# Optimization experiments

Hardware: AMD Instinct MI355X
Metric: run time of the kernel (lower is better)

The kernel has to match this reference:

```python
import jax, jax.numpy as jnp
import numpy as np

B, N, D, H, CD = 1, 512, 256, 8, 3
HD = D // H
HID = int(D * 4.0 * (2.0 / 3.0))  # 682, SwiGLU hidden


def _ln(x, w, b, eps=1e-5):
    mu = jnp.mean(x, axis=-1, keepdims=True)
    var = jnp.var(x, axis=-1, keepdims=True)
    return (x - mu) / jnp.sqrt(var + eps) * w + b


def setup_inputs() -> dict:
    key = jax.random.key(0)
    ks = jax.random.split(key, 24)
    g = lambda i, shape, fan: jax.random.normal(ks[i], shape, jnp.float32) * (1.0 / np.sqrt(fan))
    return {
        "x": jax.random.normal(ks[0], (B, N, D), jnp.float32),
        "coords": jax.random.normal(ks[1], (B, N, CD), jnp.float32),
        "ln1_w": jnp.ones((D,), jnp.float32), "ln1_b": jnp.zeros((D,), jnp.float32),
        "ln2_w": jnp.ones((D,), jnp.float32), "ln2_b": jnp.zeros((D,), jnp.float32),
        "qkv_w": g(2, (3 * D, D), D), "qkv_b": jnp.zeros((3 * D,), jnp.float32),
        "rb1_w": g(3, (D, CD), CD), "rb1_b": jnp.zeros((D,), jnp.float32),
        "rb2_w": g(4, (H, D), D), "rb2_b": jnp.zeros((H,), jnp.float32),
        "rv1_w": g(5, (D, CD), CD), "rv1_b": jnp.zeros((D,), jnp.float32),
        "rv2_w": g(6, (D, D), D), "rv2_b": jnp.zeros((D,), jnp.float32),
        "ffn_w1": g(7, (HID, D), D), "ffn_b1": jnp.zeros((HID,), jnp.float32),
        "ffn_w2": g(8, (HID, D), D), "ffn_b2": jnp.zeros((HID,), jnp.float32),
        "ffn_w3": g(9, (D, HID), HID), "ffn_b3": jnp.zeros((D,), jnp.float32),
    }


def _forward(x, coords, ln1_w, ln1_b, ln2_w, ln2_b, qkv_w, qkv_b,
             rb1_w, rb1_b, rb2_w, rb2_b, rv1_w, rv1_b, rv2_w, rv2_b,
             ffn_w1, ffn_b1, ffn_w2, ffn_b2, ffn_w3, ffn_b3):
    silu = jax.nn.silu
    xn = _ln(x, ln1_w, ln1_b)
    qkv = xn @ qkv_w.T + qkv_b                       # [B,N,3D]
    q, k, v = jnp.split(qkv, 3, axis=-1)
    tohead = lambda t: t.reshape(B, N, H, HD).transpose(0, 2, 1, 3)  # [B,H,N,hd]
    qh, kh, vh = tohead(q), tohead(k), tohead(v)

    rel = coords[:, :, None, :] - coords[:, None, :, :]              # [B,N,N,3]
    rel_bias = silu(rel @ rb1_w.T + rb1_b) @ rb2_w.T + rb2_b         # [B,N,N,H]
    rel_bias = rel_bias.transpose(0, 3, 1, 2)                        # [B,H,N,N]
    rel_value = silu(rel @ rv1_w.T + rv1_b) @ rv2_w.T + rv2_b        # [B,N,N,D]
    rel_value = rel_value.reshape(B, N, N, H, HD).transpose(0, 3, 1, 2, 4)  # [B,H,N,N,hd]

    scores = jnp.einsum('bhid,bhjd->bhij', qh, kh) / np.sqrt(float(HD))
    weights = jax.nn.softmax(scores + rel_bias, axis=-1)             # [B,H,N,N]
    context = jnp.einsum('bhij,bhjd->bhid', weights, vh) \
            + jnp.einsum('bhij,bhijd->bhid', weights, rel_value)
    attn_out = context.transpose(0, 2, 1, 3).reshape(B, N, D)

    x = x + attn_out
    xn2 = _ln(x, ln2_w, ln2_b)
    ffn = (silu(xn2 @ ffn_w1.T + ffn_b1) * (xn2 @ ffn_w2.T + ffn_b2)) @ ffn_w3.T + ffn_b3
    return x + ffn


def reference(x, coords, ln1_w, ln1_b, ln2_w, ln2_b, qkv_w, qkv_b,
              rb1_w, rb1_b, rb2_w, rb2_b, rv1_w, rv1_b, rv2_w, rv2_b,
              ffn_w1, ffn_b1, ffn_w2, ffn_b2, ffn_w3, ffn_b3):
    return _forward(x, coords, ln1_w, ln1_b, ln2_w, ln2_b, qkv_w, qkv_b,
                    rb1_w, rb1_b, rb2_w, rb2_b, rv1_w, rv1_b, rv2_w, rv2_b,
                    ffn_w1, ffn_b1, ffn_w2, ffn_b2, ffn_w3, ffn_b3)
```

## Files before the change

kernel.cpp:

```cpp
#include <hip/hip_runtime.h>


#define NN 512
#define DD 256
#define HH 8
#define HIDN 682
#define QKSCALE 0.17677669529663687f

#define OFF_QB    0
#define OFF_PB    65536
#define OFF_X2    0
#define OFF_KF    131072
#define OFF_RB2F  196608
#define OFF_XN2   131072
#define OFF_RV2F  262144
#define OFF_VT    294912
#define OFF_PV    360448
#define OFF_WB    425984
#define OFF_XN    425984
#define OFF_QKVP  557056
#define OFF_W12P  425984
#define OFF_W3P   775168
#define OFF_H1    949760

typedef float  f32x4  __attribute__((ext_vector_type(4)));
typedef short  bf16x8 __attribute__((ext_vector_type(8)));
typedef __fp16 fp16x2 __attribute__((ext_vector_type(2)));
typedef unsigned int u32;

static __device__ __forceinline__ float wredSum(float v){
#pragma unroll
  for (int o = 1; o < 64; o <<= 1) v += __shfl_xor(v, o, 64);
  return v;
}
static __device__ __forceinline__ float wredMax(float v){
#pragma unroll
  for (int o = 1; o < 64; o <<= 1) v = fmaxf(v, __shfl_xor(v, o, 64));
  return v;
}
static __device__ __forceinline__ float fsilu(float x){
  return x * __builtin_amdgcn_rcpf(1.0f + __expf(-x));
}
static __device__ __forceinline__ u32 cvtpk(float lo, float hi){
  u32 d; asm("v_cvt_pk_bf16_f32 %0, %1, %2" : "=v"(d) : "v"(lo), "v"(hi));
  return d;
}
static __device__ __forceinline__ u32 pkf16(float lo, float hi){
  fp16x2 r = __builtin_amdgcn_cvt_pkrtz(lo, hi);
  union{fp16x2 h; u32 u;} c; c.h = r; return c.u;
}
static __device__ __forceinline__ float f16lo(u32 d){
  union{unsigned short s; __fp16 h;} c; c.s = (unsigned short)(d & 0xffffu); return (float)c.h;
}
static __device__ __forceinline__ float f16hi(u32 d){
  union{unsigned short s; __fp16 h;} c; c.s = (unsigned short)(d >> 16); return (float)c.h;
}
static __device__ __forceinline__ bf16x8 mkfrag(u32 a, u32 b, u32 c, u32 d){
  union{u32 u[4]; bf16x8 s;} f; f.u[0]=a; f.u[1]=b; f.u[2]=c; f.u[3]=d; return f.s;
}
static __device__ __forceinline__ float dot4(float4 a, float4 b){
  return a.x*b.x + a.y*b.y + a.z*b.z + a.w*b.w;
}

__global__ __launch_bounds__(256) void k1_prep(
    const float* __restrict__ x, const float* __restrict__ coords,
    const float* __restrict__ ln1_w, const float* __restrict__ ln1_b,
    const float* __restrict__ rb1_w, const float* __restrict__ rv1_w,
    const float* __restrict__ rv2_w, const float* __restrict__ rb2_w,
    const float* __restrict__ qkv_w, float* __restrict__ ws)
{
  __shared__ float r4[4];
  const int b = blockIdx.x, t = threadIdx.x;
  if (b < 512) {
    const int lane = t & 63, wid = t >> 6;
    const float v = x[b*DD + t];
    float s = wredSum(v);
    if (lane == 0) r4[wid] = s;
    __syncthreads();
    const float mu = (r4[0]+r4[1]+r4[2]+r4[3]) * (1.0f/DD);
    const float d = v - mu;
    float s2 = wredSum(d*d);
    __syncthreads();
    if (lane == 0) r4[wid] = s2;
    __syncthreads();
    const float var = (r4[0]+r4[1]+r4[2]+r4[3]) * (1.0f/DD);
    ws[OFF_XN + b*DD + t] = d*rsqrtf(var + 1e-5f)*ln1_w[t] + ln1_b[t];
  } else if (b < 528) {
    u32* PB32 = (u32*)(ws + OFF_PB);
#pragma unroll
    for (int k = 0; k < 4; ++k) {
      const int L = (b-512)*1024 + k*256 + t;
      const int jt = L >> 9, ks = (L >> 6) & 7, ln = L & 63;
      const int lmm = ln & 15, lgg = ln >> 4;
      const int j = jt*16 + lmm, e0 = ks*32 + lgg*8;
      const float c0 = coords[j*3], c1 = coords[j*3+1], c2 = coords[j*3+2];
      float p[8];
#pragma unroll
      for (int r = 0; r < 8; ++r)
        p[r] = c0*rb1_w[(e0+r)*3] + c1*rb1_w[(e0+r)*3+1] + c2*rb1_w[(e0+r)*3+2];
      uint4 q; q.x = pkf16(p[0],p[1]); q.y = pkf16(p[2],p[3]);
      q.z = pkf16(p[4],p[5]); q.w = pkf16(p[6],p[7]);
      *(uint4*)(PB32 + (size_t)L*4) = q;
    }
  } else if (b < 544) {
    u32* PV32 = (u32*)(ws + OFF_PV);
#pragma unroll
    for (int k = 0; k < 4; ++k) {
      const int L = (b-528)*1024 + k*256 + t;
      const int et = L >> 10, ks = (L >> 6) & 15, ln = L & 63;
      const int lmm = ln & 15, lgg = ln >> 4;
      const int e = et*16 + lmm, j0 = ks*32 + lgg*8;
      const float w0 = rv1_w[e*3], w1 = rv1_w[e*3+1], w2 = rv1_w[e*3+2];
      float p[8];
#pragma unroll
      for (int r = 0; r < 8; ++r)
        p[r] = coords[(j0+r)*3]*w0 + coords[(j0+r)*3+1]*w1 + coords[(j0+r)*3+2]*w2;
      uint4 q; q.x = pkf16(p[0],p[1]); q.y = pkf16(p[2],p[3]);
      q.z = pkf16(p[4],p[5]); q.w = pkf16(p[6],p[7]);
      *(uint4*)(PV32 + (size_t)L*4) = q;
    }
  } else if (b < 552) {
    u32* RV32 = (u32*)(ws + OFF_RV2F);
#pragma unroll
    for (int k = 0; k < 4; ++k) {
      const int L = (b-544)*1024 + k*256 + t;
      const int mt = L >> 9, ks2 = (L >> 6) & 7, ln = L & 63;
      const int lmm = ln & 15, lgg = ln >> 4;
      const int c = mt*16 + lmm, e0 = ks2*32 + lgg*8;
      const float4 f0 = *(const float4*)(rv2_w + c*DD + e0);
      const float4 f1 = *(const float4*)(rv2_w + c*DD + e0 + 4);
      uint4 q; q.x = cvtpk(f0.x,f0.y); q.y = cvtpk(f0.z,f0.w);
      q.z = cvtpk(f1.x,f1.y); q.w = cvtpk(f1.z,f1.w);
      *(uint4*)(RV32 + (size_t)L*4) = q;
    }
  } else if (b == 552) {
    u32* RBF = (u32*)(ws + OFF_RB2F);
    const int l = t & 63, lmm = l & 15, lgg = (l >> 4) & 3, kq = t >> 6;
#pragma unroll
    for (int g = 0; g < 2; ++g) {
      const int ks = g*4 + kq;
      u32 dw[4];
#pragma unroll
      for (int dd = 0; dd < 4; ++dd) {
        const int e0 = ks*32 + lgg*8 + 2*dd;
        const float f0 = (lmm < HH) ? rb2_w[lmm*DD + e0]     : 0.f;
        const float f1 = (lmm < HH) ? rb2_w[lmm*DD + e0 + 1] : 0.f;
        dw[dd] = cvtpk(f0, f1);
      }
      uint4 q4; q4.x = dw[0]; q4.y = dw[1]; q4.z = dw[2]; q4.w = dw[3];
      *(uint4*)(RBF + (ks*64 + l)*4) = q4;
    }
  } else {
    float4* dst = (float4*)(ws + OFF_QKVP);
#pragma unroll
    for (int k = 0; k < 4; ++k) {
      const int L4 = (b - 553)*1024 + k*256 + t;
      const int O = L4 % 768, k4 = L4 / 768;
      dst[L4] = *(const float4*)(qkv_w + O*DD + k4*4);
    }
  }
}

__global__ __launch_bounds__(256) void k2_qkv(
    float* __restrict__ ws, const float* __restrict__ qkv_b)
{
  const int i0 = blockIdx.x*2, rep = blockIdx.y, t = threadIdx.x;
  const int O = rep*DD + t;
  const float4* xn4 = (const float4*)(ws + OFF_XN);
  const float4* wp4 = (const float4*)(ws + OFF_QKVP);
  float a0 = qkv_b[O], a1 = a0;
  for (int k4 = 0; k4 < 64; ++k4) {
    const float4 w = wp4[k4*768 + O];
    const float4 x0 = xn4[i0*64 + k4];
    const float4 x1 = xn4[i0*64 + 64 + k4];
    a0 += dot4(x0, w);
    a1 += dot4(x1, w);
  }
  if (rep == 0) {
    u32* QB = (u32*)(ws + OFF_QB);
    const float s0 = a0*QKSCALE, s1 = a1*QKSCALE;
    const float p0 = __shfl_xor(s0, 1);
    const float p1 = __shfl_xor(s1, 1);
    if ((t & 1) == 0) {
      QB[i0*128 + (t >> 1)]     = cvtpk(s0, p0);
      QB[(i0+1)*128 + (t >> 1)] = cvtpk(s1, p1);
    }
  } else if (rep == 1) {
    u32* KF = (u32*)(ws + OFF_KF);
    const float p0 = __shfl_xor(a0, 1);
    const float p1 = __shfl_xor(a1, 1);
    if ((t & 1) == 0) {
      const int hq = t >> 5, lgk = (t >> 3) & 3, dw = (t & 7) >> 1;
      const int jt0_ = i0 >> 4, lm0 = i0 & 15;
      KF[(((jt0_*8 + hq)*4 + lgk)*16 + lm0)*4 + dw] = cvtpk(a0, p0);
      const int j1 = i0 + 1, jt1_ = j1 >> 4, lm1 = j1 & 15;
      KF[(((jt1_*8 + hq)*4 + lgk)*16 + lm1)*4 + dw] = cvtpk(a1, p1);
    }
  } else {
    u32* VT = (u32*)(ws + OFF_VT);
    VT[t*256 + (i0 >> 1)] = cvtpk(a0, a1);
  }
}

__global__ __launch_bounds__(256, 2) void k3a_scores(
    const float* __restrict__ coords, const float* __restrict__ rb1_w,
    const float* __restrict__ rb1_b, float* __restrict__ ws)
{
  __shared__ __align__(16) float aI4[4][DD];
  __shared__ __align__(16) float eI4[4][DD];
  const int bx = blockIdx.x, t = threadIdx.x;
  const int it = bx >> 2, jq = bx & 3, i0 = it*4;
  const int lane = t & 63, w = t >> 6, lm = lane & 15, lg = lane >> 4;
  {
    const float w0 = rb1_w[t*3], w1 = rb1_w[t*3+1], w2 = rb1_w[t*3+2], bb = rb1_b[t];
#pragma unroll
    for (int i = 0; i < 4; ++i) {
      const float a = coords[(i0+i)*3]*w0 + coords[(i0+i)*3+1]*w1
                    + coords[(i0+i)*3+2]*w2 + bb;
      aI4[i][t] = a; eI4[i][t] = __expf(-a);
    }
  }
  __syncthreads();
  const uint4* PBu = (const uint4*)(ws + OFF_PB);
  const uint4* KFu = (const uint4*)(ws + OFF_KF);
  const uint4* QBu = (const uint4*)(ws + OFF_QB);
  const u32*   RBF = (const u32*)(ws + OFF_RB2F);
  const int jtA = jq*8 + w*2;
  f32x4 z = {0,0,0,0};
  f32x4 acc[2][4] = {{z,z,z,z},{z,z,z,z}};
  for (int ks = 0; ks < 8; ++ks) {
    const uint4 bd = *(const uint4*)(RBF + (ks*64 + lane)*4);
    const bf16x8 bfr = mkfrag(bd.x,bd.y,bd.z,bd.w);
    float4 aA[4][2], eA[4][2];
#pragma unroll
    for (int i = 0; i < 4; ++i) {
      aA[i][0] = *(const float4*)&aI4[i][ks*32 + lg*8];
      aA[i][1] = *(const float4*)&aI4[i][ks*32 + lg*8 + 4];
      eA[i][0] = *(const float4*)&eI4[i][ks*32 + lg*8];
      eA[i][1] = *(const float4*)&eI4[i][ks*32 + lg*8 + 4];
    }
#pragma unroll
    for (int j2 = 0; j2 < 2; ++j2) {
      const uint4 pd = PBu[((jtA+j2)*8 + ks)*64 + lane];
      float p[8], ep[8];
      p[0]=f16lo(pd.x); p[1]=f16hi(pd.x); p[2]=f16lo(pd.y); p[3]=f16hi(pd.y);
      p[4]=f16lo(pd.z); p[5]=f16hi(pd.z); p[6]=f16lo(pd.w); p[7]=f16hi(pd.w);
#pragma unroll
      for (int r = 0; r < 8; ++r) ep[r] = __expf(p[r]);
#pragma unroll
      for (int i = 0; i < 4; ++i) {
        const float* aa = (const float*)&aA[i][0];
        const float* ee = (const float*)&eA[i][0];
        float s[8];
#pragma unroll
        for (int r = 0; r < 8; ++r)
          s[r] = (aa[r] - p[r]) * __builtin_amdgcn_rcpf(fmaf(ee[r], ep[r], 1.f));
        const bf16x8 afr = mkfrag(cvtpk(s[0],s[1]), cvtpk(s[2],s[3]),
                                  cvtpk(s[4],s[5]), cvtpk(s[6],s[7]));
        acc[j2][i] = __builtin_amdgcn_mfma_f32_16x16x32_bf16(afr, bfr, acc[j2][i], 0,0,0);
      }
    }
  }
#pragma unroll
  for (int hq = 0; hq < 8; ++hq) {
    uint4 qd[4];
#pragma unroll
    for (int i = 0; i < 4; ++i) qd[i] = QBu[(i0+i)*32 + hq*4 + lg];
    const bool sel = (lm == hq);
#pragma unroll
    for (int j2 = 0; j2 < 2; ++j2) {
      const uint4 kd = KFu[((jtA+j2)*8 + hq)*64 + lane];
      const bf16x8 kfr = mkfrag(kd.x,kd.y,kd.z,kd.w);
#pragma unroll
      for (int i = 0; i < 4; ++i) {
        const bf16x8 qfr = mkfrag(sel?qd[i].x:0u, sel?qd[i].y:0u,
                                  sel?qd[i].z:0u, sel?qd[i].w:0u);
        acc[j2][i] = __builtin_amdgcn_mfma_f32_16x16x32_bf16(kfr, qfr, acc[j2][i], 0,0,0);
      }
    }
  }
  u32* WB = (u32*)(ws + OFF_WB);
  if (lm < HH) {
#pragma unroll
    for (int j2 = 0; j2 < 2; ++j2) {
      const int jt = jtA + j2, j0 = jt*16 + lg*4;
      const int ksw = j0 >> 5, rr = j0 & 31, lgw = rr >> 3, d0 = (rr & 7) >> 1;
#pragma unroll
      for (int i = 0; i < 4; ++i) {
        const int idx = (((i0+i)*16 + ksw)*32 + lgw*8 + lm)*4 + d0;
        uint2 st; st.x = pkf16(acc[j2][i][0], acc[j2][i][1]);
        st.y = pkf16(acc[j2][i][2], acc[j2][i][3]);
        *(uint2*)(WB + idx) = st;
      }
    }
  }
}

__global__ __launch_bounds__(256) void k3b_softmax(float* __restrict__ ws)
{
  const int i = blockIdx.x, t = threadIdx.x;
  const int lane = t & 63, w4 = t >> 6;
  u32* WB = (u32*)(ws + OFF_WB);
  const int ks = lane >> 2, d = lane & 3;
#pragma unroll
  for (int hh = 0; hh < 2; ++hh) {
    const int h = w4 + hh*4;
    u32 dv[4]; float v[8];
#pragma unroll
    for (int lg = 0; lg < 4; ++lg) {
      dv[lg] = WB[(i*16 + ks)*128 + (lg*8 + h)*4 + d];
      v[lg*2]   = f16lo(dv[lg]);
      v[lg*2+1] = f16hi(dv[lg]);
    }
    float m = v[0];
#pragma unroll
    for (int r = 1; r < 8; ++r) m = fmaxf(m, v[r]);
    m = wredMax(m);
    float s = 0.f;
#pragma unroll
    for (int r = 0; r < 8; ++r) { v[r] = __expf(v[r] - m); s += v[r]; }
    s = wredSum(s);
    const float rz = __builtin_amdgcn_rcpf(s);
#pragma unroll
    for (int lg = 0; lg < 4; ++lg)
      WB[(i*16 + ks)*128 + (lg*8 + h)*4 + d] = cvtpk(v[lg*2]*rz, v[lg*2+1]*rz);
  }
}

__global__ __launch_bounds__(512, 2) void k3c_ctx(
    const float* __restrict__ x, const float* __restrict__ coords,
    const float* __restrict__ rv1_w, const float* __restrict__ rv1_b,
    const float* __restrict__ rv2_b, const float* __restrict__ ln2_w,
    const float* __restrict__ ln2_b, float* __restrict__ ws)
{
  __shared__ __align__(16) float aV2[2][DD];
  __shared__ __align__(16) float eV2[2][DD];
  __shared__ __align__(16) float Gs[2][HH][260];
  __shared__ __align__(16) float x2t[2][257];
  __shared__ float red[2][4];
  const int bx = blockIdx.x, t = threadIdx.x, i0 = bx*2;
  const int lane = t & 63, w = t >> 6, lm = lane & 15, lg = lane >> 4;
  {
    const int ii = t >> 8, e = t & 255;
    const float pv = coords[(i0+ii)*3]*rv1_w[e*3] + coords[(i0+ii)*3+1]*rv1_w[e*3+1]
                   + coords[(i0+ii)*3+2]*rv1_w[e*3+2] + rv1_b[e];
    aV2[ii][e] = pv; eV2[ii][e] = __expf(-pv);
  }
  __syncthreads();
  const uint4* WBu = (const uint4*)(ws + OFF_WB);
  const uint4* PVu = (const uint4*)(ws + OFF_PV);
  const uint4* VTu = (const uint4*)(ws + OFF_VT);
  const uint4* RVu = (const uint4*)(ws + OFF_RV2F);
  f32x4 z = {0,0,0,0};
  f32x4 accg[2][2] = {{z,z},{z,z}};
  f32x4 ac1[2] = {z,z};
  float aV[2][2], eV[2][2];
#pragma unroll
  for (int e2 = 0; e2 < 2; ++e2)
#pragma unroll
    for (int ig = 0; ig < 2; ++ig) {
      aV[e2][ig] = aV2[ig][(w*2+e2)*16 + lm];
      eV[e2][ig] = eV2[ig][(w*2+e2)*16 + lm];
    }
  for (int ks = 0; ks < 16; ++ks) {
    bf16x8 wfr[2];
#pragma unroll
    for (int ig = 0; ig < 2; ++ig) {
      const uint4 wd = WBu[((i0+ig)*16 + ks)*32 + lg*8 + lm];
      wfr[ig] = mkfrag(wd.x,wd.y,wd.z,wd.w);
    }
    const uint4 cd = WBu[((i0+lm)*16 + ks)*32 + lg*8 + w];
    const bf16x8 c1b = mkfrag(cd.x,cd.y,cd.z,cd.w);
#pragma unroll
    for (int e2 = 0; e2 < 2; ++e2) {
      const int et = w*2 + e2;
      const uint4 pd = PVu[(et*16 + ks)*64 + lane];
      float p[8], ep[8];
      p[0]=f16lo(pd.x); p[1]=f16hi(pd.x); p[2]=f16lo(pd.y); p[3]=f16hi(pd.y);
      p[4]=f16lo(pd.z); p[5]=f16hi(pd.z); p[6]=f16lo(pd.w); p[7]=f16hi(pd.w);
#pragma unroll
      for (int r = 0; r < 8; ++r) ep[r] = __expf(p[r]);
#pragma unroll
      for (int ig = 0; ig < 2; ++ig) {
        float s[8];
#pragma unroll
        for (int r = 0; r < 8; ++r)
          s[r] = (aV[e2][ig] - p[r]) * __builtin_amdgcn_rcpf(fmaf(eV[e2][ig], ep[r], 1.f));
        const bf16x8 afr = mkfrag(cvtpk(s[0],s[1]), cvtpk(s[2],s[3]),
                                  cvtpk(s[4],s[5]), cvtpk(s[6],s[7]));
        accg[e2][ig] = __builtin_amdgcn_mfma_f32_16x16x32_bf16(afr, wfr[ig], accg[e2][ig], 0,0,0);
      }
    }
#pragma unroll
    for (int m2 = 0; m2 < 2; ++m2) {
      const int c = (w*2 + m2)*16 + lm;
      const uint4 vd = VTu[c*64 + ks*4 + lg];
      const bf16x8 vfr = mkfrag(vd.x,vd.y,vd.z,vd.w);
      ac1[m2] = __builtin_amdgcn_mfma_f32_16x16x32_bf16(vfr, c1b, ac1[m2], 0,0,0);
    }
  }
  if (lm < HH) {
#pragma unroll
    for (int e2 = 0; e2 < 2; ++e2)
#pragma unroll
      for (int ig = 0; ig < 2; ++ig)
#pragma unroll
        for (int g = 0; g < 4; ++g)
          Gs[ig][lm][(w*2+e2)*16 + lg*4 + g] = accg[e2][ig][g];
  }
  __syncthreads();
  f32x4 ac2[2] = {z,z};
  const int il = lm & 1;
  for (int k2 = 0; k2 < 8; ++k2) {
    const float4 g0 = *(const float4*)&Gs[il][w][k2*32 + lg*8];
    const float4 g1 = *(const float4*)&Gs[il][w][k2*32 + lg*8 + 4];
    const bf16x8 gfr = mkfrag(cvtpk(g0.x,g0.y), cvtpk(g0.z,g0.w),
                              cvtpk(g1.x,g1.y), cvtpk(g1.z,g1.w));
#pragma unroll
    for (int m2 = 0; m2 < 2; ++m2) {
      const uint4 ad = RVu[((w*2+m2)*8 + k2)*64 + lane];
      const bf16x8 afr = mkfrag(ad.x,ad.y,ad.z,ad.w);
      ac2[m2] = __builtin_amdgcn_mfma_f32_16x16x32_bf16(afr, gfr, ac2[m2], 0,0,0);
    }
  }
#pragma unroll
  for (int m2 = 0; m2 < 2; ++m2) {
    const int c0 = (w*2 + m2)*16 + lg*4;
    const float4 rb = *(const float4*)(rv2_b + c0);
    if (lm < 2) {
      const float4 xv = *(const float4*)(x + (i0+lm)*DD + c0);
      x2t[lm][c0+0] = ac1[m2][0] + ac2[m2][0] + rb.x + xv.x;
      x2t[lm][c0+1] = ac1[m2][1] + ac2[m2][1] + rb.y + xv.y;
      x2t[lm][c0+2] = ac1[m2][2] + ac2[m2][2] + rb.z + xv.z;
      x2t[lm][c0+3] = ac1[m2][3] + ac2[m2][3] + rb.w + xv.w;
    }
  }
  __syncthreads();
  const int ii = t >> 8, c = t & 255;
  const float v = x2t[ii][c];
  float s1 = wredSum(v);
  if (lane == 0) red[ii][w & 3] = s1;
  __syncthreads();
  const float mu = (red[ii][0]+red[ii][1]+red[ii][2]+red[ii][3]) * (1.0f/DD);
  const float dv = v - mu;
  float s2 = wredSum(dv*dv);
  __syncthreads();
  if (lane == 0) red[ii][w & 3] = s2;
  __syncthreads();
  const float var = (red[ii][0]+red[ii][1]+red[ii][2]+red[ii][3]) * (1.0f/DD);
  const float rstd = rsqrtf(var + 1e-5f);
  ws[OFF_X2  + (i0+ii)*DD + c] = v;
  ws[OFF_XN2 + (i0+ii)*DD + c] = dv*rstd*ln2_w[c] + ln2_b[c];
}

__global__ __launch_bounds__(256) void k3p_pack(
    const float* __restrict__ w1, const float* __restrict__ w2,
    const float* __restrict__ w3, float* __restrict__ ws)
{
  const int b = blockIdx.x, t = threadIdx.x;
  if (b < 88) {
    float4* dst = (float4*)(ws + OFF_W12P);
    for (int L4 = b*256 + t; L4 < 87296; L4 += 88*256) {
      const int pr = L4 & 1, rest = L4 >> 1;
      const int O = rest % 682, k4 = rest / 682;
      dst[L4] = *(const float4*)((pr ? w2 : w1) + O*DD + k4*4);
    }
  } else {
    float2* dst = (float2*)(ws + OFF_W3P);
    for (int L2 = (b-88)*256 + t; L2 < 87296; L2 += 44*256) {
      const int c = L2 & 255, k2i = L2 >> 8;
      dst[L2] = *(const float2*)(w3 + c*HIDN + 2*k2i);
    }
  }
}

__global__ __launch_bounds__(256) void k4_ffn1(
    float* __restrict__ ws, const float* __restrict__ b1, const float* __restrict__ b2)
{
  __shared__ __align__(16) float xr[4][DD];
  const int i0 = blockIdx.x*4, rep = blockIdx.y, t = threadIdx.x;
#pragma unroll
  for (int r = 0; r < 4; ++r) xr[r][t] = ws[OFF_XN2 + (i0+r)*DD + t];
  __syncthreads();
  const int O = rep*DD + t;
  if (O >= HIDN) return;
  const float4* wp4 = (const float4*)(ws + OFF_W12P);
  float a1[4], a2[4];
  const float bb1 = b1[O], bb2 = b2[O];
#pragma unroll
  for (int r = 0; r < 4; ++r) { a1[r] = bb1; a2[r] = bb2; }
  for (int k4 = 0; k4 < 64; ++k4) {
    const float4 u = wp4[(k4*HIDN + O)*2];
    const float4 v = wp4[(k4*HIDN + O)*2 + 1];
#pragma unroll
    for (int r = 0; r < 4; ++r) {
      const float4 xv = *(const float4*)&xr[r][k4*4];
      a1[r] += dot4(xv, u); a2[r] += dot4(xv, v);
    }
  }
#pragma unroll
  for (int r = 0; r < 4; ++r)
    ws[OFF_H1 + (size_t)(i0+r)*HIDN + O] = fsilu(a1[r]) * a2[r];
}

__global__ __launch_bounds__(256) void k5_ffn2(
    const float* __restrict__ ws, const float* __restrict__ b3, float* __restrict__ out)
{
  __shared__ __align__(16) float hr[2][HIDN + 2];
  const int i0 = blockIdx.x*2, c = threadIdx.x;
#pragma unroll
  for (int r = 0; r < 2; ++r)
    for (int e = c; e < HIDN; e += 256)
      hr[r][e] = ws[OFF_H1 + (size_t)(i0+r)*HIDN + e];
  __syncthreads();
  const float2* wp2 = (const float2*)(ws + OFF_W3P);
  float acc0 = b3[c] + ws[OFF_X2 + i0*DD + c];
  float acc1 = b3[c] + ws[OFF_X2 + (i0+1)*DD + c];
  for (int k = 0; k < 341; ++k) {
    const float2 wv = wp2[k*DD + c];
    const float2 h0 = *(const float2*)&hr[0][2*k];
    const float2 h1 = *(const float2*)&hr[1][2*k];
    acc0 += h0.x*wv.x + h0.y*wv.y;
    acc1 += h1.x*wv.x + h1.y*wv.y;
  }
  out[i0*DD + c] = acc0;
  out[(i0+1)*DD + c] = acc1;
}

extern "C" void kernel_launch(void* const* d_in, const int* in_sizes, int n_in,
                              void* d_out, int out_size, void* d_ws, size_t ws_size,
                              hipStream_t stream) {
  (void)in_sizes; (void)n_in; (void)out_size; (void)ws_size;
  const float* x      = (const float*)d_in[0];
  const float* coords = (const float*)d_in[1];
  const float* ln1_w  = (const float*)d_in[2];
  const float* ln1_b  = (const float*)d_in[3];
  const float* ln2_w  = (const float*)d_in[4];
  const float* ln2_b  = (const float*)d_in[5];
  const float* qkv_w  = (const float*)d_in[6];
  const float* qkv_b  = (const float*)d_in[7];
  const float* rb1_w  = (const float*)d_in[8];
  const float* rb1_b  = (const float*)d_in[9];
  const float* rb2_w  = (const float*)d_in[10];
  const float* rv1_w  = (const float*)d_in[12];
  const float* rv1_b  = (const float*)d_in[13];
  const float* rv2_w  = (const float*)d_in[14];
  const float* rv2_b  = (const float*)d_in[15];
  const float* ffn_w1 = (const float*)d_in[16];
  const float* ffn_b1 = (const float*)d_in[17];
  const float* ffn_w2 = (const float*)d_in[18];
  const float* ffn_b2 = (const float*)d_in[19];
  const float* ffn_w3 = (const float*)d_in[20];
  const float* ffn_b3 = (const float*)d_in[21];
  float* ws  = (float*)d_ws;
  float* out = (float*)d_out;

  k1_prep<<<601, 256, 0, stream>>>(x, coords, ln1_w, ln1_b, rb1_w, rv1_w,
                                   rv2_w, rb2_w, qkv_w, ws);
  k2_qkv<<<dim3(256, 3), 256, 0, stream>>>(ws, qkv_b);
  k3a_scores<<<512, 256, 0, stream>>>(coords, rb1_w, rb1_b, ws);
  k3b_softmax<<<512, 256, 0, stream>>>(ws);
  k3c_ctx<<<256, 512, 0, stream>>>(x, coords, rv1_w, rv1_b, rv2_b, ln2_w, ln2_b, ws);
  k3p_pack<<<132, 256, 0, stream>>>(ffn_w1, ffn_w2, ffn_w3, ws);
  k4_ffn1<<<dim3(128, 3), 256, 0, stream>>>(ws, ffn_b1, ffn_b2);
  k5_ffn2<<<256, 256, 0, stream>>>(ws, ffn_b3, out);
}
```

Baseline: 209.0 us.

## Pack QKV and FFN weights as bf16 in prep kernel, drop separate pack kernel

Weights for the QKV projection and the three FFN matrices are converted to bf16 inside the first prep kernel, which replaces the separate FFN pack kernel and removes one launch. The QKV and FFN matmul kernels now read bf16 weights, halving their weight traffic, and unpack them to fp32 for FMA. QKV now handles 4 rows per block staged in shared memory, and FFN1 handles 8 rows per block, so each weight load is reused across more rows. The trade-offs are bf16 rounding of the weights, which may affect accuracy, and a reworked workspace layout that moves several buffers to new offsets.

```diff
diff --git a/kernel.cpp b/kernel.cpp
--- a/kernel.cpp
+++ b/kernel.cpp
@@ -9,19 +9,19 @@
 
 #define OFF_QB    0
 #define OFF_PB    65536
-#define OFF_X2    0
 #define OFF_KF    131072
 #define OFF_RB2F  196608
-#define OFF_XN2   131072
-#define OFF_RV2F  262144
-#define OFF_VT    294912
-#define OFF_PV    360448
-#define OFF_WB    425984
-#define OFF_XN    425984
-#define OFF_QKVP  557056
-#define OFF_W12P  425984
-#define OFF_W3P   775168
-#define OFF_H1    949760
+#define OFF_RV2F  198656
+#define OFF_VT    231424
+#define OFF_PV    296960
+#define OFF_WB    362496
+#define OFF_XN    1443904
+#define OFF_X2    1574976
+#define OFF_XN2   1706048
+#define OFF_H1    1837120
+#define OFF_QKVPB 2186304
+#define OFF_W12B  2284608
+#define OFF_W3B   2459200
 
 typedef float  f32x4  __attribute__((ext_vector_type(4)));
 typedef short  bf16x8 __attribute__((ext_vector_type(8)));
@@ -55,11 +55,14 @@
 static __device__ __forceinline__ float f16hi(u32 d){
   union{unsigned short s; __fp16 h;} c; c.s = (unsigned short)(d >> 16); return (float)c.h;
 }
+static __device__ __forceinline__ float bflo(u32 u){
+  union{u32 v; float f;} c; c.v = u << 16; return c.f;
+}
+static __device__ __forceinline__ float bfhi(u32 u){
+  union{u32 v; float f;} c; c.v = u & 0xffff0000u; return c.f;
+}
 static __device__ __forceinline__ bf16x8 mkfrag(u32 a, u32 b, u32 c, u32 d){
   union{u32 u[4]; bf16x8 s;} f; f.u[0]=a; f.u[1]=b; f.u[2]=c; f.u[3]=d; return f.s;
-}
-static __device__ __forceinline__ float dot4(float4 a, float4 b){
-  return a.x*b.x + a.y*b.y + a.z*b.z + a.w*b.w;
 }
 
 __global__ __launch_bounds__(256) void k1_prep(
@@ -67,7 +70,9 @@
     const float* __restrict__ ln1_w, const float* __restrict__ ln1_b,
     const float* __restrict__ rb1_w, const float* __restrict__ rv1_w,
     const float* __restrict__ rv2_w, const float* __restrict__ rb2_w,
-    const float* __restrict__ qkv_w, float* __restrict__ ws)
+    const float* __restrict__ qkv_w, const float* __restrict__ w1,
+    const float* __restrict__ w2, const float* __restrict__ w3,
+    float* __restrict__ ws)
 {
   __shared__ float r4[4];
   const int b = blockIdx.x, t = threadIdx.x;
@@ -110,11 +115,11 @@
       const int et = L >> 10, ks = (L >> 6) & 15, ln = L & 63;
       const int lmm = ln & 15, lgg = ln >> 4;
       const int e = et*16 + lmm, j0 = ks*32 + lgg*8;
-      const float w0 = rv1_w[e*3], w1 = rv1_w[e*3+1], w2 = rv1_w[e*3+2];
+      const float w0 = rv1_w[e*3], w1_ = rv1_w[e*3+1], w2_ = rv1_w[e*3+2];
       float p[8];
 #pragma unroll
       for (int r = 0; r < 8; ++r)
-        p[r] = coords[(j0+r)*3]*w0 + coords[(j0+r)*3+1]*w1 + coords[(j0+r)*3+2]*w2;
+        p[r] = coords[(j0+r)*3]*w0 + coords[(j0+r)*3+1]*w1_ + coords[(j0+r)*3+2]*w2_;
       uint4 q; q.x = pkf16(p[0],p[1]); q.y = pkf16(p[2],p[3]);
       q.z = pkf16(p[4],p[5]); q.w = pkf16(p[6],p[7]);
       *(uint4*)(PV32 + (size_t)L*4) = q;
@@ -150,13 +155,44 @@
       uint4 q4; q4.x = dw[0]; q4.y = dw[1]; q4.z = dw[2]; q4.w = dw[3];
       *(uint4*)(RBF + (ks*64 + l)*4) = q4;
     }
+  } else if (b < 601) {
+    uint2* qp = (uint2*)(ws + OFF_QKVPB);
+#pragma unroll
+    for (int k = 0; k < 4; ++k) {
+      const int idx = (b-553)*1024 + k*256 + t;
+      const int O = idx % 768, kp = idx / 768;
+      const float4 wv = *(const float4*)(qkv_w + O*DD + kp*4);
+      uint2 u; u.x = cvtpk(wv.x, wv.y); u.y = cvtpk(wv.z, wv.w);
+      qp[idx] = u;
+    }
+  } else if (b < 687) {
+    uint2* wp = (uint2*)(ws + OFF_W12B);
+#pragma unroll
+    for (int k = 0; k < 4; ++k) {
+      const int idx = (b-601)*1024 + k*256 + t;
+      if (idx < 87296) {
+        const int m = idx & 1, r2 = idx >> 1;
+        const int O = r2 % HIDN, kp = r2 / HIDN;
+        const float4 wv = *(const float4*)((m ? w2 : w1) + O*DD + kp*4);
+        uint2 u; u.x = cvtpk(wv.x, wv.y); u.y = cvtpk(wv.z, wv.w);
+        wp[idx] = u;
+      }
+    }
   } else {
-    float4* dst = (float4*)(ws + OFF_QKVP);
+    uint2* wp = (uint2*)(ws + OFF_W3B);
 #pragma unroll
     for (int k = 0; k < 4; ++k) {
-      const int L4 = (b - 553)*1024 + k*256 + t;
-      const int O = L4 % 768, k4 = L4 / 768;
-      dst[L4] = *(const float4*)(qkv_w + O*DD + k4*4);
+      const int idx = (b-687)*1024 + k*256 + t;
+      if (idx < 43776) {
+        const int c = idx % 256, kq = idx / 256;
+        const int k0 = kq*4;
+        const float v0 = w3[c*HIDN + k0];
+        const float v1 = w3[c*HIDN + k0 + 1];
+        const float v2 = (k0+2 < HIDN) ? w3[c*HIDN + k0 + 2] : 0.f;
+        const float v3 = (k0+3 < HIDN) ? w3[c*HIDN + k0 + 3] : 0.f;
+        uint2 u; u.x = cvtpk(v0, v1); u.y = cvtpk(v2, v3);
+        wp[idx] = u;
+      }
     }
   }
 }
@@ -164,41 +200,50 @@
 __global__ __launch_bounds__(256) void k2_qkv(
     float* __restrict__ ws, const float* __restrict__ qkv_b)
 {
-  const int i0 = blockIdx.x*2, rep = blockIdx.y, t = threadIdx.x;
+  __shared__ __align__(16) float xr[4][DD];
+  const int i0 = blockIdx.x*4, rep = blockIdx.y, t = threadIdx.x;
+#pragma unroll
+  for (int r = 0; r < 4; ++r) xr[r][t] = ws[OFF_XN + (i0+r)*DD + t];
+  __syncthreads();
   const int O = rep*DD + t;
-  const float4* xn4 = (const float4*)(ws + OFF_XN);
-  const float4* wp4 = (const float4*)(ws + OFF_QKVP);
-  float a0 = qkv_b[O], a1 = a0;
-  for (int k4 = 0; k4 < 64; ++k4) {
-    const float4 w = wp4[k4*768 + O];
-    const float4 x0 = xn4[i0*64 + k4];
-    const float4 x1 = xn4[i0*64 + 64 + k4];
-    a0 += dot4(x0, w);
-    a1 += dot4(x1, w);
+  const uint2* wq = (const uint2*)(ws + OFF_QKVPB);
+  float a[4];
+  const float bb = qkv_b[O];
+#pragma unroll
+  for (int r = 0; r < 4; ++r) a[r] = bb;
+  for (int kp = 0; kp < 64; ++kp) {
+    const uint2 u = wq[kp*768 + O];
+    const float w0 = bflo(u.x), w1 = bfhi(u.x), w2 = bflo(u.y), w3v = bfhi(u.y);
+#pragma unroll
+    for (int r = 0; r < 4; ++r) {
+      const float4 xv = *(const float4*)&xr[r][kp*4];
+      a[r] += xv.x*w0 + xv.y*w1 + xv.z*w2 + xv.w*w3v;
+    }
   }
   if (rep == 0) {
     u32* QB = (u32*)(ws + OFF_QB);
-    const float s0 = a0*QKSCALE, s1 = a1*QKSCALE;
-    const float p0 = __shfl_xor(s0, 1);
-    const float p1 = __shfl_xor(s1, 1);
-    if ((t & 1) == 0) {
-      QB[i0*128 + (t >> 1)]     = cvtpk(s0, p0);
-      QB[(i0+1)*128 + (t >> 1)] = cvtpk(s1, p1);
+#pragma unroll
+    for (int r = 0; r < 4; ++r) {
+      const float s = a[r]*QKSCALE;
+      const float p = __shfl_xor(s, 1);
+      if ((t & 1) == 0) QB[(i0+r)*128 + (t >> 1)] = cvtpk(s, p);
     }
   } else if (rep == 1) {
     u32* KF = (u32*)(ws + OFF_KF);
-    const float p0 = __shfl_xor(a0, 1);
-    const float p1 = __shfl_xor(a1, 1);
-    if ((t & 1) == 0) {
-      const int hq = t >> 5, lgk = (t >> 3) & 3, dw = (t & 7) >> 1;
-      const int jt0_ = i0 >> 4, lm0 = i0 & 15;
-      KF[(((jt0_*8 + hq)*4 + lgk)*16 + lm0)*4 + dw] = cvtpk(a0, p0);
-      const int j1 = i0 + 1, jt1_ = j1 >> 4, lm1 = j1 & 15;
-      KF[(((jt1_*8 + hq)*4 + lgk)*16 + lm1)*4 + dw] = cvtpk(a1, p1);
+#pragma unroll
+    for (int r = 0; r < 4; ++r) {
+      const float p = __shfl_xor(a[r], 1);
+      if ((t & 1) == 0) {
+        const int hq = t >> 5, lgk = (t >> 3) & 3, dw = (t & 7) >> 1;
+        const int j = i0 + r, jt = j >> 4, lmr = j & 15;
+        KF[(((jt*8 + hq)*4 + lgk)*16 + lmr)*4 + dw] = cvtpk(a[r], p);
+      }
     }
   } else {
     u32* VT = (u32*)(ws + OFF_VT);
-    VT[t*256 + (i0 >> 1)] = cvtpk(a0, a1);
+#pragma unroll
+    for (int rp = 0; rp < 2; ++rp)
+      VT[t*256 + (i0 >> 1) + rp] = cvtpk(a[2*rp], a[2*rp+1]);
   }
 }
 
@@ -453,75 +498,58 @@
   ws[OFF_XN2 + (i0+ii)*DD + c] = dv*rstd*ln2_w[c] + ln2_b[c];
 }
 
-__global__ __launch_bounds__(256) void k3p_pack(
-    const float* __restrict__ w1, const float* __restrict__ w2,
-    const float* __restrict__ w3, float* __restrict__ ws)
-{
-  const int b = blockIdx.x, t = threadIdx.x;
-  if (b < 88) {
-    float4* dst = (float4*)(ws + OFF_W12P);
-    for (int L4 = b*256 + t; L4 < 87296; L4 += 88*256) {
-      const int pr = L4 & 1, rest = L4 >> 1;
-      const int O = rest % 682, k4 = rest / 682;
-      dst[L4] = *(const float4*)((pr ? w2 : w1) + O*DD + k4*4);
-    }
-  } else {
-    float2* dst = (float2*)(ws + OFF_W3P);
-    for (int L2 = (b-88)*256 + t; L2 < 87296; L2 += 44*256) {
-      const int c = L2 & 255, k2i = L2 >> 8;
-      dst[L2] = *(const float2*)(w3 + c*HIDN + 2*k2i);
-    }
-  }
-}
-
 __global__ __launch_bounds__(256) void k4_ffn1(
     float* __restrict__ ws, const float* __restrict__ b1, const float* __restrict__ b2)
 {
-  __shared__ __align__(16) float xr[4][DD];
-  const int i0 = blockIdx.x*4, rep = blockIdx.y, t = threadIdx.x;
-#pragma unroll
-  for (int r = 0; r < 4; ++r) xr[r][t] = ws[OFF_XN2 + (i0+r)*DD + t];
+  __shared__ __align__(16) float xr[8][DD];
+  const int i0 = blockIdx.x*8, rep = blockIdx.y, t = threadIdx.x;
+#pragma unroll
+  for (int r = 0; r < 8; ++r) xr[r][t] = ws[OFF_XN2 + (i0+r)*DD + t];
   __syncthreads();
   const int O = rep*DD + t;
   if (O >= HIDN) return;
-  const float4* wp4 = (const float4*)(ws + OFF_W12P);
-  float a1[4], a2[4];
+  const uint2* wp = (const uint2*)(ws + OFF_W12B);
+  float a1[8], a2[8];
   const float bb1 = b1[O], bb2 = b2[O];
 #pragma unroll
-  for (int r = 0; r < 4; ++r) { a1[r] = bb1; a2[r] = bb2; }
-  for (int k4 = 0; k4 < 64; ++k4) {
-    const float4 u = wp4[(k4*HIDN + O)*2];
-    const float4 v = wp4[(k4*HIDN + O)*2 + 1];
-#pragma unroll
-    for (int r = 0; r < 4; ++r) {
-      const float4 xv = *(const float4*)&xr[r][k4*4];
-      a1[r] += dot4(xv, u); a2[r] += dot4(xv, v);
-    }
-  }
-#pragma unroll
-  for (int r = 0; r < 4; ++r)
+  for (int r = 0; r < 8; ++r) { a1[r] = bb1; a2[r] = bb2; }
+  for (int kp = 0; kp < 64; ++kp) {
+    const uint2 u1 = wp[(kp*HIDN + O)*2];
+    const uint2 u2 = wp[(kp*HIDN + O)*2 + 1];
+    const float u10=bflo(u1.x), u11=bfhi(u1.x), u12=bflo(u1.y), u13=bfhi(u1.y);
+    const float u20=bflo(u2.x), u21=bfhi(u2.x), u22=bflo(u2.y), u23=bfhi(u2.y);
+#pragma unroll
+    for (int r = 0; r < 8; ++r) {
+      const float4 xv = *(const float4*)&xr[r][kp*4];
+      a1[r] += xv.x*u10 + xv.y*u11 + xv.z*u12 + xv.w*u13;
+      a2[r] += xv.x*u20 + xv.y*u21 + xv.z*u22 + xv.w*u23;
+    }
+  }
+#pragma unroll
+  for (int r = 0; r < 8; ++r)
     ws[OFF_H1 + (size_t)(i0+r)*HIDN + O] = fsilu(a1[r]) * a2[r];
 }
 
 __global__ __launch_bounds__(256) void k5_ffn2(
     const float* __restrict__ ws, const float* __restrict__ b3, float* __restrict__ out)
 {
-  __shared__ __align__(16) float hr[2][HIDN + 2];
+  __shared__ __align__(16) float hr[2][684];
   const int i0 = blockIdx.x*2, c = threadIdx.x;
 #pragma unroll
   for (int r = 0; r < 2; ++r)
-    for (int e = c; e < HIDN; e += 256)
-      hr[r][e] = ws[OFF_H1 + (size_t)(i0+r)*HIDN + e];
-  __syncthreads();
-  const float2* wp2 = (const float2*)(ws + OFF_W3P);
+    for (int e = c; e < 684; e += 256)
+      hr[r][e] = (e < HIDN) ? ws[OFF_H1 + (size_t)(i0+r)*HIDN + e] : 0.f;
+  __syncthreads();
+  const uint2* wp = (const uint2*)(ws + OFF_W3B);
   float acc0 = b3[c] + ws[OFF_X2 + i0*DD + c];
   float acc1 = b3[c] + ws[OFF_X2 + (i0+1)*DD + c];
-  for (int k = 0; k < 341; ++k) {
-    const float2 wv = wp2[k*DD + c];
-    const float2 h0 = *(const float2*)&hr[0][2*k];
-    const float2 h1 = *(const float2*)&hr[1][2*k];
-    acc0 += h0.x*wv.x + h0.y*wv.y;
-    acc1 += h1.x*wv.x + h1.y*wv.y;
+  for (int kq = 0; kq < 171; ++kq) {
+    const uint2 u = wp[kq*256 + c];
+    const float w0 = bflo(u.x), w1 = bfhi(u.x), w2 = bflo(u.y), w3v = bfhi(u.y);
+    const float4 h0 = *(const float4*)&hr[0][kq*4];
+    const float4 h1 = *(const float4*)&hr[1][kq*4];
+    acc0 += h0.x*w0 + h0.y*w1 + h0.z*w2 + h0.w*w3v;
+    acc1 += h1.x*w0 + h1.y*w1 + h1.z*w2 + h1.w*w3v;
   }
   out[i0*DD + c] = acc0;
   out[(i0+1)*DD + c] = acc1;
@@ -555,13 +583,12 @@
   float* ws  = (float*)d_ws;
   float* out = (float*)d_out;
 
-  k1_prep<<<601, 256, 0, stream>>>(x, coords, ln1_w, ln1_b, rb1_w, rv1_w,
-                                   rv2_w, rb2_w, qkv_w, ws);
-  k2_qkv<<<dim3(256, 3), 256, 0, stream>>>(ws, qkv_b);
+  k1_prep<<<730, 256, 0, stream>>>(x, coords, ln1_w, ln1_b, rb1_w, rv1_w,
+                                   rv2_w, rb2_w, qkv_w, ffn_w1, ffn_w2, ffn_w3, ws);
+  k2_qkv<<<dim3(128, 3), 256, 0, stream>>>(ws, qkv_b);
   k3a_scores<<<512, 256, 0, stream>>>(coords, rb1_w, rb1_b, ws);
   k3b_softmax<<<512, 256, 0, stream>>>(ws);
   k3c_ctx<<<256, 512, 0, stream>>>(x, coords, rv1_w, rv1_b, rv2_b, ln2_w, ln2_b, ws);
-  k3p_pack<<<132, 256, 0, stream>>>(ffn_w1, ffn_w2, ffn_w3, ws);
-  k4_ffn1<<<dim3(128, 3), 256, 0, stream>>>(ws, ffn_b1, ffn_b2);
+  k4_ffn1<<<dim3(64, 3), 256, 0, stream>>>(ws, ffn_b1, ffn_b2);
   k5_ffn2<<<256, 256, 0, stream>>>(ws, ffn_b3, out);
 }
```

New measurement: 227.8 us. 9.0% more time.
